# Performance work log

Hardware: AMD Instinct MI355X
Metric: run time of the kernel (lower is better)

Reference implementation:

```python
import jax, jax.numpy as jnp
import numpy as np

INP_DIM, OUT_DIM, MID_DIM, MID_LAYERS = 3, 1, 4, 2


def _uniform(key, shape, bound):
    return jax.random.uniform(key, shape, jnp.float32, -bound, bound)


def setup_inputs() -> dict:
    key = jax.random.key(0)
    ks = jax.random.split(key, 16)
    B, T = 4096, 1024
    bnd = 1.0 / np.sqrt(MID_DIM)  # PyTorch LSTM/Linear init bound
    d = {
        "x": jax.random.normal(ks[0], (B, T, INP_DIM), jnp.float32),
        # layer 0 LSTM (gate order i,f,g,o stacked along rows)
        "W_ih0": _uniform(ks[1], (4 * MID_DIM, INP_DIM), bnd),
        "W_hh0": _uniform(ks[2], (4 * MID_DIM, MID_DIM), bnd),
        "b_ih0": _uniform(ks[3], (4 * MID_DIM,), bnd),
        "b_hh0": _uniform(ks[4], (4 * MID_DIM,), bnd),
        # layer 1 LSTM
        "W_ih1": _uniform(ks[5], (4 * MID_DIM, MID_DIM), bnd),
        "W_hh1": _uniform(ks[6], (4 * MID_DIM, MID_DIM), bnd),
        "b_ih1": _uniform(ks[7], (4 * MID_DIM,), bnd),
        "b_hh1": _uniform(ks[8], (4 * MID_DIM,), bnd),
        "W1": _uniform(ks[9], (MID_DIM, MID_DIM), bnd),
        "b1": _uniform(ks[10], (MID_DIM,), bnd),
        "W2": _uniform(ks[11], (OUT_DIM, MID_DIM), bnd),
        "b2": _uniform(ks[12], (OUT_DIM,), bnd),
    }
    return d


def _lstm_layer(x_tbd, W_ih, W_hh, b_ih, b_hh):
    # x_tbd: [T, B, D] time-major. Precompute input contribution to all gates.
    H = W_hh.shape[1]
    xg = jnp.einsum("tbd,gd->tbg", x_tbd, W_ih) + (b_ih + b_hh)  # [T,B,4H]

    def step(carry, xg_t):
        h, c = carry
        g = xg_t + h @ W_hh.T  # [B,4H]
        i, f, gg, o = jnp.split(g, 4, axis=-1)
        i = jax.nn.sigmoid(i)
        f = jax.nn.sigmoid(f)
        gg = jnp.tanh(gg)
        o = jax.nn.sigmoid(o)
        c = f * c + i * gg
        h = o * jnp.tanh(c)
        return (h, c), h

    B = x_tbd.shape[1]
    init = (jnp.zeros((B, H), x_tbd.dtype), jnp.zeros((B, H), x_tbd.dtype))
    _, hs = jax.lax.scan(step, init, xg)
    return hs  # [T,B,H]


def reference(x, W_ih0, W_hh0, b_ih0, b_hh0, W_ih1, W_hh1, b_ih1, b_hh1, W1, b1, W2, b2):
    # x: [B,T,3] (batch_first). Run 2-layer LSTM then per-timestep MLP head.
    h = jnp.transpose(x, (1, 0, 2))  # -> [T,B,3]
    h = _lstm_layer(h, W_ih0, W_hh0, b_ih0, b_hh0)
    h = _lstm_layer(h, W_ih1, W_hh1, b_ih1, b_hh1)
    h = jnp.transpose(h, (1, 0, 2))  # -> [B,T,H]
    y = jnp.tanh(h @ W1.T + b1) @ W2.T + b2  # [B,T,1]
    return y
```

## Files before the change

### kernel.cpp

```cpp
#include <hip/hip_runtime.h>


#define T_STEPS 1024
#define BATCH   4096
#define CHUNK   16
#define NCHUNK  (T_STEPS / CHUNK)

__device__ __forceinline__ float fast_exp2(float x) {
#if __has_builtin(__builtin_amdgcn_exp2f)
    return __builtin_amdgcn_exp2f(x);
#else
    return exp2f(x);
#endif
}

__device__ __forceinline__ float fast_rcp(float x) {
#if __has_builtin(__builtin_amdgcn_rcpf)
    return __builtin_amdgcn_rcpf(x);
#else
    return 1.0f / x;
#endif
}

__device__ __forceinline__ float fast_tanh(float x) {
    return 2.0f * fast_rcp(1.0f + fast_exp2(-2.88539008f * x)) - 1.0f;
}

template <int CTRL>
__device__ __forceinline__ float dpp_mov(float v) {
    int i = __builtin_bit_cast(int, v);
    i = __builtin_amdgcn_mov_dpp(i, CTRL, 0xF, 0xF, true);
    return __builtin_bit_cast(float, i);
}

#define DPP_QB0         0x00
#define DPP_QB1         0x55
#define DPP_QB2         0xAA
#define DPP_QB3         0xFF
#define DPP_ROR8        0x128
#define DPP_MIRROR      0x140
#define DPP_HALF_MIRROR 0x141

__global__ __launch_bounds__(512) void lstm_r7_kernel(
    const float* __restrict__ x,
    const float* __restrict__ W_ih0, const float* __restrict__ W_hh0,
    const float* __restrict__ b_ih0, const float* __restrict__ b_hh0,
    const float* __restrict__ W_ih1, const float* __restrict__ W_hh1,
    const float* __restrict__ b_ih1, const float* __restrict__ b_hh1,
    const float* __restrict__ W1, const float* __restrict__ b1,
    const float* __restrict__ W2, const float* __restrict__ b2,
    float* __restrict__ out)
{
    __shared__ float4 xstage[4][2][68];
    __shared__ float4 ring[4][2][CHUNK][4];

    const int tid  = threadIdx.x;
    const int wave = tid >> 6;
    const int stg  = wave >> 2;
    const int pr   = wave & 3;
    const int lane = tid & 63;
    const int idx  = lane & 15;
    const int rho  = lane & 3;
    const int u    = (lane >> 2) & 3;
    const int r    = rho * 4 + u;
    const int ch   = lane >> 4;
    const int batch = blockIdx.x * 16 + pr * 4 + ch;

    const float am = (rho == 2) ? -2.88539008f : -1.44269504f;
    const float aa = (rho == 2) ? 2.0f : 1.0f;
    const float ab = (rho == 2) ? -1.0f : 0.0f;

    const float wx0 = W_ih0[r * 3 + 0];
    const float wx1 = W_ih0[r * 3 + 1];
    const float wx2 = W_ih0[r * 3 + 2];
    const float bias0 = b_ih0[r] + b_hh0[r];
    float wh0[4];
#pragma unroll
    for (int k = 0; k < 4; ++k) wh0[k] = W_hh0[r * 4 + (u ^ k)];

    const float bias1 = b_ih1[r] + b_hh1[r];
    float wi1[4], wh1[4], w1p[4];
#pragma unroll
    for (int k = 0; k < 4; ++k) {
        wi1[k] = W_ih1[r * 4 + k];
        wh1[k] = W_hh1[r * 4 + (u ^ k)];
        w1p[k] = W1[u * 4 + (u ^ k)];
    }
    const float b1u = b1[u];
    const float w2u = W2[u];
    const float b2v = b2[0];

    float h0 = 0.f, c0 = 0.f, h0b = 0.f, h0c = 0.f, h0d = 0.f;
    float h1 = 0.f, c1 = 0.f, h1b = 0.f, h1c = 0.f, h1d = 0.f;
    float ysave = 0.f;
    float* op = out + (size_t)batch * T_STEPS;

    const float* xrow = x + (size_t)batch * T_STEPS * 3;
    float q0 = 0.f, q1 = 0.f, q2 = 0.f;
    if (stg == 0) {
        const float* p0 = xrow + idx * 3;
        xstage[pr][0][ch * 17 + idx] = make_float4(p0[0], p0[1], p0[2], 0.f);
        const float* p1 = xrow + 48 + idx * 3;
        q0 = p1[0]; q1 = p1[1]; q2 = p1[2];
    }

    for (int c = 0; c <= NCHUNK; ++c) {
        if (stg == 0) {
            if (c < NCHUNK) {
                const int s = c & 1;
                const float4* xs = &xstage[pr][s][ch * 17];
                float4 xc = xs[0];
#pragma unroll
                for (int tt = 0; tt < CHUNK; ++tt) {
                    float4 xn = xs[(tt < CHUNK - 1) ? tt + 1 : tt];

                    float pre0 = bias0 + wx0 * xc.x + wx1 * xc.y + wx2 * xc.z
                               + wh0[0] * h0 + wh0[1] * h0b + wh0[2] * h0c + wh0[3] * h0d;
                    float a0 = aa * fast_rcp(1.0f + fast_exp2(am * pre0)) + ab;
                    float gi = dpp_mov<DPP_QB0>(a0);
                    float gf = dpp_mov<DPP_QB1>(a0);
                    float gg = dpp_mov<DPP_QB2>(a0);
                    float go = dpp_mov<DPP_QB3>(a0);
                    c0 = gf * c0 + gi * gg;
                    h0 = go * fast_tanh(c0);
                    h0b = dpp_mov<DPP_HALF_MIRROR>(h0);
                    h0c = dpp_mov<DPP_ROR8>(h0);
                    h0d = dpp_mov<DPP_MIRROR>(h0);

                    if (rho == 0) ((float*)&ring[pr][s][tt][ch])[u] = h0;
                    xc = xn;
                }
                if (c < NCHUNK - 1)
                    xstage[pr][(c + 1) & 1][ch * 17 + idx] = make_float4(q0, q1, q2, 0.f);
                if (c < NCHUNK - 2) {
                    const float* p = xrow + (c + 2) * 48 + idx * 3;
                    q0 = p[0]; q1 = p[1]; q2 = p[2];
                }
            }
        } else if (c >= 1) {
            const int cc = c - 1;
            const int s = cc & 1;
            const float4* rgp = &ring[pr][s][0][ch];
            float4 h_a = rgp[0];
            float4 h_b = rgp[4];
#pragma unroll
            for (int tt = 0; tt < CHUNK; ++tt) {
                float4 h_n = rgp[4 * ((tt < CHUNK - 2) ? tt + 2 : CHUNK - 1)];

                float pre1 = bias1
                           + wi1[0] * h_a.x + wi1[1] * h_a.y
                           + wi1[2] * h_a.z + wi1[3] * h_a.w
                           + wh1[0] * h1 + wh1[1] * h1b + wh1[2] * h1c + wh1[3] * h1d;
                float a1 = aa * fast_rcp(1.0f + fast_exp2(am * pre1)) + ab;
                float gi1 = dpp_mov<DPP_QB0>(a1);
                float gf1 = dpp_mov<DPP_QB1>(a1);
                float gg1 = dpp_mov<DPP_QB2>(a1);
                float go1 = dpp_mov<DPP_QB3>(a1);
                c1 = gf1 * c1 + gi1 * gg1;
                h1 = go1 * fast_tanh(c1);
                h1b = dpp_mov<DPP_HALF_MIRROR>(h1);
                h1c = dpp_mov<DPP_ROR8>(h1);
                h1d = dpp_mov<DPP_MIRROR>(h1);

                float zp = b1u + w1p[0] * h1 + w1p[1] * h1b + w1p[2] * h1c + w1p[3] * h1d;
                float z  = fast_tanh(zp);
                float yv = w2u * z;
                float t1 = yv + dpp_mov<DPP_ROR8>(yv);
                float y  = t1 + dpp_mov<DPP_MIRROR>(t1) + b2v;

                ysave = (tt == idx) ? y : ysave;
                h_a = h_b; h_b = h_n;
            }
            op[cc * CHUNK + idx] = ysave;
        }
        __syncthreads();
    }
}

extern "C" void kernel_launch(void* const* d_in, const int* in_sizes, int n_in,
                              void* d_out, int out_size, void* d_ws, size_t ws_size,
                              hipStream_t stream) {
    const float* x     = (const float*)d_in[0];
    const float* W_ih0 = (const float*)d_in[1];
    const float* W_hh0 = (const float*)d_in[2];
    const float* b_ih0 = (const float*)d_in[3];
    const float* b_hh0 = (const float*)d_in[4];
    const float* W_ih1 = (const float*)d_in[5];
    const float* W_hh1 = (const float*)d_in[6];
    const float* b_ih1 = (const float*)d_in[7];
    const float* b_hh1 = (const float*)d_in[8];
    const float* W1    = (const float*)d_in[9];
    const float* b1    = (const float*)d_in[10];
    const float* W2    = (const float*)d_in[11];
    const float* b2    = (const float*)d_in[12];
    float* out = (float*)d_out;

    dim3 grid(BATCH / 16);
    dim3 block(512);
    lstm_r7_kernel<<<grid, block, 0, stream>>>(
        x, W_ih0, W_hh0, b_ih0, b_hh0, W_ih1, W_hh1, b_ih1, b_hh1,
        W1, b1, W2, b2, out);
}
```

Before: 252.4 us.

## Replace block-wide barriers with per-pair LDS flag handshake and deeper ring

Each chunk used to end with a __syncthreads across all eight waves. Now each layer-0/layer-1 wave pair synchronises through done/free flags in shared memory, polled with s_sleep. The ring buffer grows from two to four chunk slots so the producer can run ahead of the consumer. This removes lockstep coupling between independent wave pairs and between the two stages. The cost is spin polling and reliance on volatile LDS flags plus block-scope fences for correct ordering.

After: 247.4 us. 2.0% less time.

```diff
diff --git a/kernel.cpp b/kernel.cpp
--- a/kernel.cpp
+++ b/kernel.cpp
@@ -5,6 +5,7 @@
 #define BATCH   4096
 #define CHUNK   16
 #define NCHUNK  (T_STEPS / CHUNK)
+#define RDEPTH  4
 
 __device__ __forceinline__ float fast_exp2(float x) {
 #if __has_builtin(__builtin_amdgcn_exp2f)
@@ -41,7 +42,7 @@
 #define DPP_MIRROR      0x140
 #define DPP_HALF_MIRROR 0x141
 
-__global__ __launch_bounds__(512) void lstm_r7_kernel(
+__global__ __launch_bounds__(512) void lstm_r8_kernel(
     const float* __restrict__ x,
     const float* __restrict__ W_ih0, const float* __restrict__ W_hh0,
     const float* __restrict__ b_ih0, const float* __restrict__ b_hh0,
@@ -52,7 +53,9 @@
     float* __restrict__ out)
 {
     __shared__ float4 xstage[4][2][68];
-    __shared__ float4 ring[4][2][CHUNK][4];
+    __shared__ float4 ring[4][RDEPTH][CHUNK][4];
+    __shared__ int done_flag[4][RDEPTH];
+    __shared__ int free_flag[4][RDEPTH];
 
     const int tid  = threadIdx.x;
     const int wave = tid >> 6;
@@ -66,80 +69,97 @@
     const int ch   = lane >> 4;
     const int batch = blockIdx.x * 16 + pr * 4 + ch;
 
+    if (tid < 4 * RDEPTH) {
+        done_flag[tid >> 2][tid & 3] = 0;
+        free_flag[tid >> 2][tid & 3] = 0;
+    }
+    __syncthreads();
+
     const float am = (rho == 2) ? -2.88539008f : -1.44269504f;
     const float aa = (rho == 2) ? 2.0f : 1.0f;
     const float ab = (rho == 2) ? -1.0f : 0.0f;
 
-    const float wx0 = W_ih0[r * 3 + 0];
-    const float wx1 = W_ih0[r * 3 + 1];
-    const float wx2 = W_ih0[r * 3 + 2];
-    const float bias0 = b_ih0[r] + b_hh0[r];
-    float wh0[4];
-#pragma unroll
-    for (int k = 0; k < 4; ++k) wh0[k] = W_hh0[r * 4 + (u ^ k)];
-
-    const float bias1 = b_ih1[r] + b_hh1[r];
-    float wi1[4], wh1[4], w1p[4];
-#pragma unroll
-    for (int k = 0; k < 4; ++k) {
-        wi1[k] = W_ih1[r * 4 + k];
-        wh1[k] = W_hh1[r * 4 + (u ^ k)];
-        w1p[k] = W1[u * 4 + (u ^ k)];
-    }
-    const float b1u = b1[u];
-    const float w2u = W2[u];
-    const float b2v = b2[0];
-
-    float h0 = 0.f, c0 = 0.f, h0b = 0.f, h0c = 0.f, h0d = 0.f;
-    float h1 = 0.f, c1 = 0.f, h1b = 0.f, h1c = 0.f, h1d = 0.f;
-    float ysave = 0.f;
-    float* op = out + (size_t)batch * T_STEPS;
-
-    const float* xrow = x + (size_t)batch * T_STEPS * 3;
-    float q0 = 0.f, q1 = 0.f, q2 = 0.f;
     if (stg == 0) {
+        const float wx0 = W_ih0[r * 3 + 0];
+        const float wx1 = W_ih0[r * 3 + 1];
+        const float wx2 = W_ih0[r * 3 + 2];
+        const float bias0 = b_ih0[r] + b_hh0[r];
+        float wh0[4];
+#pragma unroll
+        for (int k = 0; k < 4; ++k) wh0[k] = W_hh0[r * 4 + (u ^ k)];
+
+        float h0 = 0.f, c0 = 0.f, h0b = 0.f, h0c = 0.f, h0d = 0.f;
+
+        const float* xrow = x + (size_t)batch * T_STEPS * 3;
         const float* p0 = xrow + idx * 3;
         xstage[pr][0][ch * 17 + idx] = make_float4(p0[0], p0[1], p0[2], 0.f);
         const float* p1 = xrow + 48 + idx * 3;
-        q0 = p1[0]; q1 = p1[1]; q2 = p1[2];
-    }
-
-    for (int c = 0; c <= NCHUNK; ++c) {
-        if (stg == 0) {
-            if (c < NCHUNK) {
-                const int s = c & 1;
-                const float4* xs = &xstage[pr][s][ch * 17];
-                float4 xc = xs[0];
-#pragma unroll
-                for (int tt = 0; tt < CHUNK; ++tt) {
-                    float4 xn = xs[(tt < CHUNK - 1) ? tt + 1 : tt];
-
-                    float pre0 = bias0 + wx0 * xc.x + wx1 * xc.y + wx2 * xc.z
-                               + wh0[0] * h0 + wh0[1] * h0b + wh0[2] * h0c + wh0[3] * h0d;
-                    float a0 = aa * fast_rcp(1.0f + fast_exp2(am * pre0)) + ab;
-                    float gi = dpp_mov<DPP_QB0>(a0);
-                    float gf = dpp_mov<DPP_QB1>(a0);
-                    float gg = dpp_mov<DPP_QB2>(a0);
-                    float go = dpp_mov<DPP_QB3>(a0);
-                    c0 = gf * c0 + gi * gg;
-                    h0 = go * fast_tanh(c0);
-                    h0b = dpp_mov<DPP_HALF_MIRROR>(h0);
-                    h0c = dpp_mov<DPP_ROR8>(h0);
-                    h0d = dpp_mov<DPP_MIRROR>(h0);
-
-                    if (rho == 0) ((float*)&ring[pr][s][tt][ch])[u] = h0;
-                    xc = xn;
-                }
-                if (c < NCHUNK - 1)
-                    xstage[pr][(c + 1) & 1][ch * 17 + idx] = make_float4(q0, q1, q2, 0.f);
-                if (c < NCHUNK - 2) {
-                    const float* p = xrow + (c + 2) * 48 + idx * 3;
-                    q0 = p[0]; q1 = p[1]; q2 = p[2];
-                }
-            }
-        } else if (c >= 1) {
-            const int cc = c - 1;
-            const int s = cc & 1;
+        float q0 = p1[0], q1 = p1[1], q2 = p1[2];
+
+        volatile int* ff = &free_flag[pr][0];
+
+        for (int c = 0; c < NCHUNK; ++c) {
+            const int s = c & (RDEPTH - 1);
+            if (c >= RDEPTH) {
+                while (ff[s] < c - RDEPTH + 1) { __builtin_amdgcn_s_sleep(1); }
+            }
+
+            const float4* xs = &xstage[pr][c & 1][ch * 17];
+            float4 xc = xs[0];
+#pragma unroll
+            for (int tt = 0; tt < CHUNK; ++tt) {
+                float4 xn = xs[(tt < CHUNK - 1) ? tt + 1 : tt];
+
+                float pre0 = bias0 + wx0 * xc.x + wx1 * xc.y + wx2 * xc.z
+                           + wh0[0] * h0 + wh0[1] * h0b + wh0[2] * h0c + wh0[3] * h0d;
+                float a0 = aa * fast_rcp(1.0f + fast_exp2(am * pre0)) + ab;
+                float gi = dpp_mov<DPP_QB0>(a0);
+                float gf = dpp_mov<DPP_QB1>(a0);
+                float gg = dpp_mov<DPP_QB2>(a0);
+                float go = dpp_mov<DPP_QB3>(a0);
+                c0 = gf * c0 + gi * gg;
+                h0 = go * fast_tanh(c0);
+                h0b = dpp_mov<DPP_HALF_MIRROR>(h0);
+                h0c = dpp_mov<DPP_ROR8>(h0);
+                h0d = dpp_mov<DPP_MIRROR>(h0);
+
+                if (rho == 0) ((float*)&ring[pr][s][tt][ch])[u] = h0;
+                xc = xn;
+            }
+            __threadfence_block();
+            if (lane == 0) done_flag[pr][s] = c + 1;
+
+            if (c < NCHUNK - 1)
+                xstage[pr][(c + 1) & 1][ch * 17 + idx] = make_float4(q0, q1, q2, 0.f);
+            if (c < NCHUNK - 2) {
+                const float* p = xrow + (c + 2) * 48 + idx * 3;
+                q0 = p[0]; q1 = p[1]; q2 = p[2];
+            }
+        }
+    } else {
+        const float bias1 = b_ih1[r] + b_hh1[r];
+        float wi1[4], wh1[4], w1p[4];
+#pragma unroll
+        for (int k = 0; k < 4; ++k) {
+            wi1[k] = W_ih1[r * 4 + k];
+            wh1[k] = W_hh1[r * 4 + (u ^ k)];
+            w1p[k] = W1[u * 4 + (u ^ k)];
+        }
+        const float b1u = b1[u];
+        const float w2u = W2[u];
+        const float b2v = b2[0];
+
+        float h1 = 0.f, c1 = 0.f, h1b = 0.f, h1c = 0.f, h1d = 0.f;
+        float ysave = 0.f;
+        float* op = out + (size_t)batch * T_STEPS;
+
+        volatile int* df = &done_flag[pr][0];
+
+        for (int c = 0; c < NCHUNK; ++c) {
+            const int s = c & (RDEPTH - 1);
+            while (df[s] < c + 1) { __builtin_amdgcn_s_sleep(1); }
+            __threadfence_block();
+
             const float4* rgp = &ring[pr][s][0][ch];
             float4 h_a = rgp[0];
             float4 h_b = rgp[4];
@@ -171,9 +191,9 @@
                 ysave = (tt == idx) ? y : ysave;
                 h_a = h_b; h_b = h_n;
             }
-            op[cc * CHUNK + idx] = ysave;
+            if (lane == 0) free_flag[pr][s] = c + 1;
+            op[c * CHUNK + idx] = ysave;
         }
-        __syncthreads();
     }
 }
 
@@ -197,7 +217,7 @@
 
     dim3 grid(BATCH / 16);
     dim3 block(512);
-    lstm_r7_kernel<<<grid, block, 0, stream>>>(
+    lstm_r8_kernel<<<grid, block, 0, stream>>>(
         x, W_ih0, W_hh0, b_ih0, b_hh0, W_ih1, W_hh1, b_ih1, b_hh1,
         W1, b1, W2, b2, out);
 }
```
